# Kernel tuning notes

Hardware: AMD Instinct MI355X
Metric: run time of the kernel (lower is better)

Reference implementation:

```python
import jax, jax.numpy as jnp
import numpy as np

# dims: B graphs, E entities, R relations, N = E + R nodes, H hidden, P prop steps
B, N, E, R, H, P, RT, NH = 4, 2048, 1600, 448, 512, 2, 100, 4
DH = H // NH  # head dim = 128


def setup_inputs() -> dict:
    key = jax.random.key(0)
    ks = jax.random.split(key, 12)
    adj = jax.random.randint(ks[0], (B, N, N), 0, 2, dtype=jnp.int32)
    # self-loops so no attention row is fully masked (avoids NaN softmax rows)
    adj = jnp.maximum(adj, jnp.eye(N, dtype=jnp.int32)[None])
    rels = jax.random.randint(ks[1], (B, R), 0, RT, dtype=jnp.int32)
    vents = jax.random.normal(ks[2], (B, E, H), jnp.float32)
    renc_w = jax.random.normal(ks[3], (RT, H), jnp.float32) * 0.05  # xavier-ish
    s = 0.02
    inp = dict(adjs=adj, rels=rels, vents=vents, entlen=E, renc_w=renc_w)
    inp["Wq"] = jax.random.normal(ks[4], (P, H, H), jnp.float32) * s
    inp["Wk"] = jax.random.normal(ks[5], (P, H, H), jnp.float32) * s
    inp["Wv"] = jax.random.normal(ks[6], (P, H, H), jnp.float32) * s
    inp["Wo"] = jax.random.normal(ks[7], (P, H, H), jnp.float32) * s
    inp["W1"] = jax.random.normal(ks[8], (P, H, 4 * H), jnp.float32) * s
    inp["W2"] = jax.random.normal(ks[9], (P, 4 * H, H), jnp.float32) * s
    inp["bq"] = jnp.zeros((P, H), jnp.float32)
    inp["bk"] = jnp.zeros((P, H), jnp.float32)
    inp["bv"] = jnp.zeros((P, H), jnp.float32)
    inp["bo"] = jnp.zeros((P, H), jnp.float32)
    inp["b1"] = jnp.zeros((P, 4 * H), jnp.float32)
    inp["b2"] = jnp.zeros((P, H), jnp.float32)
    inp["ln1_g"] = jnp.ones((P, H), jnp.float32)
    inp["ln1_b"] = jnp.zeros((P, H), jnp.float32)
    inp["ln2_g"] = jnp.ones((P, H), jnp.float32)
    inp["ln2_b"] = jnp.zeros((P, H), jnp.float32)
    inp["prelu_a"] = jnp.full((P, 4 * H), 0.25, jnp.float32)  # torch PReLU default
    return inp


def _ln(x, g, b):
    mu = x.mean(-1, keepdims=True)
    var = x.var(-1, keepdims=True)
    return (x - mu) * jax.lax.rsqrt(var + jnp.float32(1e-5)) * g + b


def reference(adjs, rels, vents, entlen, renc_w, Wq, Wk, Wv, Wo, W1, W2,
              bq, bk, bv, bo, b1, b2, ln1_g, ln1_b, ln2_g, ln2_b, prelu_a):
    vrel = renc_w[rels]                              # (B,R,H) relation embeddings
    x = jnp.concatenate([vents, vrel], axis=1)       # (B,N,H) graph node features
    neg = (adjs == 0)[:, None, :, :]                 # (B,1,N,N) True = masked
    for j in range(P):  # prop steps, structurally distinct layers
        q = (x @ Wq[j] + bq[j]).reshape(B, N, NH, DH)
        k = (x @ Wk[j] + bk[j]).reshape(B, N, NH, DH)
        v = (x @ Wv[j] + bv[j]).reshape(B, N, NH, DH)
        sc = jnp.einsum('bqhd,bkhd->bhqk', q, k) / jnp.sqrt(jnp.float32(DH))
        sc = jnp.where(neg, jnp.float32(-1e9), sc)
        a = jax.nn.softmax(sc, axis=-1)
        o = jnp.einsum('bhqk,bkhd->bqhd', a, v).reshape(B, N, H)
        attn_out = o @ Wo[j] + bo[j]
        t = _ln(attn_out, ln1_g[j], ln1_b[j])        # ln_1
        hpre = t @ W1[j] + b1[j]
        hact = jnp.where(hpre >= 0, hpre, prelu_a[j] * hpre)  # PReLU
        y = hact @ W2[j] + b2[j]                     # dropout is identity in eval
        x = _ln(y + t, ln2_g[j], ln2_b[j])           # ln_2 residual
    glob = x[:, entlen]                              # (B,H) global node = vgraph[entlens[i]]
    gents = x                                        # (B,N,H) all graphs same size -> no pad
    elens = jnp.full((B,), N, jnp.int32)
    emask = jnp.arange(N)[None, :] <= elens[:, None] # (B,N) faithful `<=` comparison
    return glob, gents, emask
```

## Files before the change

### kernel.cpp

```cpp
#include <hip/hip_runtime.h>

typedef unsigned short u16;
typedef __bf16 bf16x8 __attribute__((ext_vector_type(8)));
typedef float floatx4 __attribute__((ext_vector_type(4)));


__device__ __forceinline__ float bf2f(u16 u) {
  union { unsigned int i; float f; } c; c.i = ((unsigned int)u) << 16; return c.f;
}
__device__ __forceinline__ u16 f2bf(float f) {
  union { unsigned int i; float f; } c; c.f = f;
  unsigned int i = c.i;
  return (u16)((i + 0x7FFFu + ((i >> 16) & 1u)) >> 16);
}

__device__ __forceinline__ void gload16(const u16* __restrict__ g, u16* l) {
  __builtin_amdgcn_global_load_lds(
      (const __attribute__((address_space(1))) unsigned int*)g,
      (__attribute__((address_space(3))) unsigned int*)l, 16, 0, 0);
}

template <int EPI, int FOUT, int SEG3>
__global__ __launch_bounds__(256, 3) void gemm_tn(
    const u16* __restrict__ A, const u16* __restrict__ Bt, void* __restrict__ Cv,
    const float* __restrict__ bias, const float* __restrict__ bias2,
    const float* __restrict__ bias3, const float* __restrict__ alpha,
    const float* __restrict__ res, int K, int lda, int ldb, int ldc) {
  __shared__ __align__(16) u16 As[2][128 * 32];
  __shared__ __align__(16) u16 Bs[2][128 * 32];

  const int tid = threadIdx.x;
  const int w = tid >> 6, lane = tid & 63;
  const int quad = lane >> 4, l16 = lane & 15;
  const int wm = w & 1, wn = w >> 1;

  const int slot0 = w * 128 + lane;
  const int slot1 = slot0 + 64;
  const u16* pA0 = A + (long)(blockIdx.x * 128 + (slot0 >> 2)) * lda + (slot0 & 3) * 8;
  const u16* pA1 = A + (long)(blockIdx.x * 128 + (slot1 >> 2)) * lda + (slot1 & 3) * 8;
  const u16* pB0 = Bt + (long)(blockIdx.y * 128 + (slot0 >> 2)) * ldb + (slot0 & 3) * 8;
  const u16* pB1 = Bt + (long)(blockIdx.y * 128 + (slot1 >> 2)) * ldb + (slot1 & 3) * 8;
  const int woff0 = w * 1024;
  const int woff1 = woff0 + 512;

  const floatx4 z4 = {0.f, 0.f, 0.f, 0.f};
  floatx4 acc[4][4];
#pragma unroll
  for (int i = 0; i < 4; i++)
#pragma unroll
    for (int j = 0; j < 4; j++) acc[i][j] = z4;

  gload16(pA0, &As[0][woff0]);
  gload16(pA1, &As[0][woff1]);
  gload16(pB0, &Bs[0][woff0]);
  gload16(pB1, &Bs[0][woff1]);
  pA0 += 32; pA1 += 32; pB0 += 32; pB1 += 32;
  __syncthreads();

  int p = 0;
  for (int k0 = 0; k0 < K; k0 += 32) {
    if (k0 + 32 < K) {
      gload16(pA0, &As[p ^ 1][woff0]);
      gload16(pA1, &As[p ^ 1][woff1]);
      gload16(pB0, &Bs[p ^ 1][woff0]);
      gload16(pB1, &Bs[p ^ 1][woff1]);
      pA0 += 32; pA1 += 32; pB0 += 32; pB1 += 32;
    }

    bf16x8 af[4], bv[4];
#pragma unroll
    for (int mi = 0; mi < 4; mi++)
      af[mi] = *(const bf16x8*)&As[p][(wm * 64 + mi * 16 + l16) * 32 + quad * 8];
#pragma unroll
    for (int ni = 0; ni < 4; ni++)
      bv[ni] = *(const bf16x8*)&Bs[p][(wn * 64 + ni * 16 + l16) * 32 + quad * 8];
#pragma unroll
    for (int mi = 0; mi < 4; mi++)
#pragma unroll
      for (int ni = 0; ni < 4; ni++)
        acc[mi][ni] = __builtin_amdgcn_mfma_f32_16x16x32_bf16(af[mi], bv[ni], acc[mi][ni], 0, 0, 0);

    __syncthreads();
    p ^= 1;
  }

  const float* bptr = bias;
  if (SEG3) {
    const int seg = blockIdx.y >> 2;
    bptr = (seg == 0) ? bias : ((seg == 1) ? bias2 : bias3);
  }
  const long crow0 = (long)blockIdx.x * 128;
  const int ncol0 = blockIdx.y * 128 + wn * 64 + l16;
#pragma unroll
  for (int mi = 0; mi < 4; mi++) {
#pragma unroll
    for (int r = 0; r < 4; r++) {
      const int m = wm * 64 + mi * 16 + quad * 4 + r;
      const long rowbase = (crow0 + m) * (long)ldc;
      const float* rrow = (EPI == 3) ? (res + rowbase) : nullptr;
#pragma unroll
      for (int ni = 0; ni < 4; ni++) {
        const int n = ncol0 + ni * 16;
        float vv = acc[mi][ni][r] + bptr[SEG3 ? (n & 511) : n];
        if (EPI == 2) { if (vv < 0.f) vv *= alpha[n]; }
        if (EPI == 3) vv += rrow[n];
        if (FOUT) ((float*)Cv)[rowbase + n] = vv;
        else ((u16*)Cv)[rowbase + n] = f2bf(vv);
      }
    }
  }
}

template <int EPI, int FOUT>
__global__ __launch_bounds__(256, 3) void gemm_tn64(
    const u16* __restrict__ A, const u16* __restrict__ Bt, void* __restrict__ Cv,
    const float* __restrict__ bias, const float* __restrict__ alpha,
    const float* __restrict__ res, int K, int lda, int ldb, int ldc) {
  __shared__ __align__(16) u16 As[2][128 * 32];
  __shared__ __align__(16) u16 Bs[2][64 * 32];

  const int tid = threadIdx.x;
  const int w = tid >> 6, lane = tid & 63;
  const int quad = lane >> 4, l16 = lane & 15;

  const int rA0 = tid >> 2, cA = (tid & 3) * 8;
  const int rA1 = rA0 + 64;
  const u16* pA0 = A + (long)(blockIdx.x * 128 + rA0) * lda + cA;
  const u16* pA1 = A + (long)(blockIdx.x * 128 + rA1) * lda + cA;
  const u16* pB  = Bt + (long)(blockIdx.y * 64 + rA0) * ldb + cA;
  const int aoff0 = w * 512;
  const int aoff1 = aoff0 + 2048;
  const int boff  = w * 512;

  const floatx4 z4 = {0.f, 0.f, 0.f, 0.f};
  floatx4 acc[2][4];
#pragma unroll
  for (int i = 0; i < 2; i++)
#pragma unroll
    for (int j = 0; j < 4; j++) acc[i][j] = z4;

  gload16(pA0, &As[0][aoff0]);
  gload16(pA1, &As[0][aoff1]);
  gload16(pB, &Bs[0][boff]);
  pA0 += 32; pA1 += 32; pB += 32;
  __syncthreads();

  int p = 0;
  for (int k0 = 0; k0 < K; k0 += 32) {
    if (k0 + 32 < K) {
      gload16(pA0, &As[p ^ 1][aoff0]);
      gload16(pA1, &As[p ^ 1][aoff1]);
      gload16(pB, &Bs[p ^ 1][boff]);
      pA0 += 32; pA1 += 32; pB += 32;
    }

    bf16x8 af[2], bv[4];
#pragma unroll
    for (int mi = 0; mi < 2; mi++)
      af[mi] = *(const bf16x8*)&As[p][(w * 32 + mi * 16 + l16) * 32 + quad * 8];
#pragma unroll
    for (int ni = 0; ni < 4; ni++)
      bv[ni] = *(const bf16x8*)&Bs[p][(ni * 16 + l16) * 32 + quad * 8];
#pragma unroll
    for (int mi = 0; mi < 2; mi++)
#pragma unroll
      for (int ni = 0; ni < 4; ni++)
        acc[mi][ni] = __builtin_amdgcn_mfma_f32_16x16x32_bf16(af[mi], bv[ni], acc[mi][ni], 0, 0, 0);

    __syncthreads();
    p ^= 1;
  }

  const long crow0 = (long)blockIdx.x * 128;
  const int ncol0 = blockIdx.y * 64 + l16;
#pragma unroll
  for (int mi = 0; mi < 2; mi++) {
#pragma unroll
    for (int r = 0; r < 4; r++) {
      const int m = w * 32 + mi * 16 + quad * 4 + r;
      const long rowbase = (crow0 + m) * (long)ldc;
      const float* rrow = (EPI == 3) ? (res + rowbase) : nullptr;
#pragma unroll
      for (int ni = 0; ni < 4; ni++) {
        const int n = ncol0 + ni * 16;
        float vv = acc[mi][ni][r] + bias[n];
        if (EPI == 2) { if (vv < 0.f) vv *= alpha[n]; }
        if (EPI == 3) vv += rrow[n];
        if (FOUT) ((float*)Cv)[rowbase + n] = vv;
        else ((u16*)Cv)[rowbase + n] = f2bf(vv);
      }
    }
  }
}

#define LDP 136
__global__ __launch_bounds__(256, 3) void k_attn(
    const u16* __restrict__ qkv, const u16* __restrict__ vt,
    const unsigned* __restrict__ mbits, u16* __restrict__ og) {
  __shared__ __align__(16) u16 KV[128 * LDP];
  __shared__ __align__(16) u16 Pl[64 * LDP];
  __shared__ unsigned Ml[64 * 4];

  const int tid = threadIdx.x;
  const int w = tid >> 6, lane = tid & 63;
  const int quad = lane >> 4, l16 = lane & 15;
  const int qt = blockIdx.x;
  const int z = blockIdx.y;
  const int b = z >> 2, h = z & 3;

  const u16* qbase = qkv + (long)b * 2048 * 1536 + h * 128;
  const u16* kbase = qbase + 512;
  const u16* vbase = vt + (long)(b * 4 + h) * 128 * 2048;
  const unsigned* mbase = mbits + ((long)b * 2048 + qt * 64) * 64;

  bf16x8 qf[4];
#pragma unroll
  for (int ks = 0; ks < 4; ks++)
    qf[ks] = *(const bf16x8*)(qbase +
        (long)(qt * 64 + w * 16 + l16) * 1536 + ks * 32 + quad * 8);

  const floatx4 z4 = {0.f, 0.f, 0.f, 0.f};
  floatx4 Oacc[8];
#pragma unroll
  for (int ni = 0; ni < 8; ni++) Oacc[ni] = z4;
  float mrow[4], lrow[4];
#pragma unroll
  for (int r = 0; r < 4; r++) { mrow[r] = -3.4e38f; lrow[r] = 0.f; }

  const float scale = 0.08838834764831845f;
  const int srow = tid >> 4;
  const int scol = (tid & 15) * 8;

  for (int kt = 0; kt < 16; kt++) {
    __syncthreads();
#pragma unroll
    for (int rr = 0; rr < 128; rr += 16)
      *(int4*)&KV[(rr + srow) * LDP + scol] =
          *(const int4*)(kbase + (long)(kt * 128 + rr + srow) * 1536 + scol);
    Ml[tid] = mbase[(tid >> 2) * 64 + kt * 4 + (tid & 3)];
    __syncthreads();

    floatx4 accS[8];
#pragma unroll
    for (int ni = 0; ni < 8; ni++) accS[ni] = z4;
#pragma unroll
    for (int ks = 0; ks < 4; ks++) {
      bf16x8 bf[8];
#pragma unroll
      for (int ni = 0; ni < 8; ni++)
        bf[ni] = *(const bf16x8*)&KV[(ni * 16 + l16) * LDP + ks * 32 + quad * 8];
#pragma unroll
      for (int ni = 0; ni < 8; ni++)
        accS[ni] = __builtin_amdgcn_mfma_f32_16x16x32_bf16(qf[ks], bf[ni], accS[ni], 0, 0, 0);
    }
    __syncthreads();

#pragma unroll
    for (int rr = 0; rr < 128; rr += 16)
      *(int4*)&KV[(rr + srow) * LDP + scol] =
          *(const int4*)(vbase + (long)(rr + srow) * 2048 + kt * 128 + scol);

#pragma unroll
    for (int r = 0; r < 4; r++) {
      const int rowl = w * 16 + quad * 4 + r;
      float s[8];
      float rmax = -1e30f;
#pragma unroll
      for (int ni = 0; ni < 8; ni++) {
        const unsigned mw = Ml[rowl * 4 + (ni >> 1)];
        const int on = (mw >> ((ni & 1) * 16 + l16)) & 1;
        s[ni] = on ? accS[ni][r] * scale : -1e30f;
        rmax = fmaxf(rmax, s[ni]);
      }
#pragma unroll
      for (int off = 1; off < 16; off <<= 1) rmax = fmaxf(rmax, __shfl_xor(rmax, off, 64));
      const float mnew = fmaxf(mrow[r], rmax);
      const float al = __expf(mrow[r] - mnew);
      float rs = 0.f;
#pragma unroll
      for (int ni = 0; ni < 8; ni++) {
        const float pp = __expf(s[ni] - mnew);
        rs += pp;
        Pl[rowl * LDP + ni * 16 + l16] = f2bf(pp);
      }
#pragma unroll
      for (int off = 1; off < 16; off <<= 1) rs += __shfl_xor(rs, off, 64);
      lrow[r] = lrow[r] * al + rs;
      mrow[r] = mnew;
#pragma unroll
      for (int ni = 0; ni < 8; ni++) Oacc[ni][r] *= al;
    }
    __syncthreads();

#pragma unroll
    for (int ks = 0; ks < 4; ks++) {
      bf16x8 bv[8];
#pragma unroll
      for (int ni = 0; ni < 8; ni++)
        bv[ni] = *(const bf16x8*)&KV[(ni * 16 + l16) * LDP + ks * 32 + quad * 8];
      bf16x8 pf = *(const bf16x8*)&Pl[(w * 16 + l16) * LDP + ks * 32 + quad * 8];
#pragma unroll
      for (int ni = 0; ni < 8; ni++)
        Oacc[ni] = __builtin_amdgcn_mfma_f32_16x16x32_bf16(pf, bv[ni], Oacc[ni], 0, 0, 0);
    }
  }

#pragma unroll
  for (int r = 0; r < 4; r++) {
    const float inv = 1.f / lrow[r];
    const long q = qt * 64 + w * 16 + quad * 4 + r;
#pragma unroll
    for (int ni = 0; ni < 8; ni++)
      og[((long)b * 2048 + q) * 512 + h * 128 + ni * 16 + l16] = f2bf(Oacc[ni][r] * inv);
  }
}

__global__ __launch_bounds__(256) void k_maskpack(const int* __restrict__ adjs,
                                                  unsigned* __restrict__ bits) {
  const int wid = blockIdx.x * 4 + (threadIdx.x >> 6);
  const int lane = threadIdx.x & 63;
  const unsigned long long bal = __ballot(adjs[(long)wid * 64 + lane] != 0);
  if (lane == 0) {
    bits[wid * 2] = (unsigned)bal;
    bits[wid * 2 + 1] = (unsigned)(bal >> 32);
  }
}

__global__ __launch_bounds__(256) void tr_w(const float* __restrict__ src, u16* __restrict__ dst,
                                            int ld_src, int ld_dst, long s_z, long d_z) {
  __shared__ u16 tile[32][33];
  src += (long)blockIdx.z * s_z;
  dst += (long)blockIdx.z * d_z;
  const int r0 = blockIdx.x << 5, c0 = blockIdx.y << 5;
  const int tx = threadIdx.x & 31, ty = threadIdx.x >> 5;
#pragma unroll
  for (int i = 0; i < 32; i += 8)
    tile[ty + i][tx] = f2bf(src[(long)(r0 + ty + i) * ld_src + c0 + tx]);
  __syncthreads();
#pragma unroll
  for (int i = 0; i < 32; i += 8)
    dst[(long)(c0 + ty + i) * ld_dst + r0 + tx] = tile[tx][ty + i];
}

__global__ __launch_bounds__(256) void tr_bf16(const u16* __restrict__ src, u16* __restrict__ dst,
                                               int ld_src, int ld_dst, int zdiv,
                                               long s_out, long s_in, long d_out, long d_in_) {
  __shared__ u16 tile[32][33];
  const int zz = blockIdx.z, zq = zz / zdiv, zr = zz % zdiv;
  src += (long)zq * s_out + (long)zr * s_in;
  dst += (long)zq * d_out + (long)zr * d_in_;
  const int r0 = blockIdx.x << 5, c0 = blockIdx.y << 5;
  const int tx = threadIdx.x & 31, ty = threadIdx.x >> 5;
#pragma unroll
  for (int i = 0; i < 32; i += 8) tile[ty + i][tx] = src[(long)(r0 + ty + i) * ld_src + c0 + tx];
  __syncthreads();
#pragma unroll
  for (int i = 0; i < 32; i += 8) dst[(long)(c0 + ty + i) * ld_dst + r0 + tx] = tile[tx][ty + i];
}

__global__ __launch_bounds__(256) void k_build_x(const float* __restrict__ vents,
                                                 const int* __restrict__ rels,
                                                 const float* __restrict__ renc,
                                                 float* __restrict__ x, u16* __restrict__ xb) {
  const long idx = (long)blockIdx.x * 256 + threadIdx.x;
  const int c = (int)(idx & 511);
  const int row = (int)(idx >> 9);
  const int b = row >> 11, n = row & 2047;
  float val;
  if (n < 1600) val = vents[((long)b * 1600 + n) * 512 + c];
  else val = renc[(long)rels[b * 448 + (n - 1600)] * 512 + c];
  x[idx] = val;
  xb[idx] = f2bf(val);
}

__global__ __launch_bounds__(256) void k_ln(const float* __restrict__ in, float* __restrict__ out,
                                            u16* __restrict__ outb,
                                            const float* __restrict__ g, const float* __restrict__ bb) {
  __shared__ float rs[256], rq[256];
  const int row = blockIdx.x, tid = threadIdx.x;
  const float* p = in + (long)row * 512;
  const float a0 = p[tid], a1 = p[tid + 256];
  rs[tid] = a0 + a1;
  rq[tid] = a0 * a0 + a1 * a1;
  __syncthreads();
  for (int s = 128; s > 0; s >>= 1) {
    if (tid < s) { rs[tid] += rs[tid + s]; rq[tid] += rq[tid + s]; }
    __syncthreads();
  }
  const float mu = rs[0] * (1.f / 512.f);
  const float var = rq[0] * (1.f / 512.f) - mu * mu;
  const float inv = 1.0f / sqrtf(var + 1e-5f);
  const float o0 = (a0 - mu) * inv * g[tid] + bb[tid];
  const float o1 = (a1 - mu) * inv * g[tid + 256] + bb[tid + 256];
  out[(long)row * 512 + tid] = o0;
  out[(long)row * 512 + tid + 256] = o1;
  outb[(long)row * 512 + tid] = f2bf(o0);
  outb[(long)row * 512 + tid + 256] = f2bf(o1);
}

__global__ __launch_bounds__(256) void k_out(const float* __restrict__ x, const int* __restrict__ entlen,
                                             float* __restrict__ out, long out_n) {
  const long idx = (long)blockIdx.x * 256 + threadIdx.x;
  if (idx >= out_n) return;
  const long G = 2048, GE = 2048 + 4194304;
  float v;
  if (idx < G) {
    const int b = (int)(idx >> 9), c = (int)(idx & 511);
    int e = entlen[0];
    if (e < 0 || e >= 2048) e = 1600;
    v = x[((long)b * 2048 + e) * 512 + c];
  } else if (idx < GE) {
    v = x[idx - G];
  } else {
    v = 1.0f;
  }
  out[idx] = v;
}

extern "C" void kernel_launch(void* const* d_in, const int* in_sizes, int n_in,
                              void* d_out, int out_size, void* d_ws, size_t ws_size,
                              hipStream_t stream) {
  const int* adjs = (const int*)d_in[0];
  const int* rels = (const int*)d_in[1];
  const float* vents = (const float*)d_in[2];
  const int* entlen = (const int*)d_in[3];
  const float* renc = (const float*)d_in[4];
  const float* Wq = (const float*)d_in[5];
  const float* Wk = (const float*)d_in[6];
  const float* Wv = (const float*)d_in[7];
  const float* Wo = (const float*)d_in[8];
  const float* W1 = (const float*)d_in[9];
  const float* W2 = (const float*)d_in[10];
  const float* bq = (const float*)d_in[11];
  const float* bk = (const float*)d_in[12];
  const float* bv = (const float*)d_in[13];
  const float* bo = (const float*)d_in[14];
  const float* b1 = (const float*)d_in[15];
  const float* b2 = (const float*)d_in[16];
  const float* ln1g = (const float*)d_in[17];
  const float* ln1b = (const float*)d_in[18];
  const float* ln2g = (const float*)d_in[19];
  const float* ln2b = (const float*)d_in[20];
  const float* prelu = (const float*)d_in[21];

  char* base = (char*)d_ws;
  float* x_f   = (float*)(base + 0);
  float* t_f   = (float*)(base + 16777216);
  float* tmp_f = (float*)(base + 33554432);
  u16* wt  = (u16*)(base + 50331648);
  u16* xb  = (u16*)(base + 62914560);
  u16* tb  = (u16*)(base + 71303168);
  u16* qkv = (u16*)(base + 79691776);
  u16* Vtb = (u16*)(base + 104857600);
  u16* ob  = (u16*)(base + 113246208);
  u16* hb  = (u16*)(base + 121634816);
  unsigned* mbits = (unsigned*)(base + 155189248);

  k_build_x<<<dim3(16384), 256, 0, stream>>>(vents, rels, renc, x_f, xb);
  k_maskpack<<<dim3(65536), 256, 0, stream>>>(adjs, mbits);

  tr_w<<<dim3(16, 16, 2), 256, 0, stream>>>(Wq, wt + 0,       512, 512, 262144L, 3145728L);
  tr_w<<<dim3(16, 16, 2), 256, 0, stream>>>(Wk, wt + 262144,  512, 512, 262144L, 3145728L);
  tr_w<<<dim3(16, 16, 2), 256, 0, stream>>>(Wv, wt + 524288,  512, 512, 262144L, 3145728L);
  tr_w<<<dim3(16, 16, 2), 256, 0, stream>>>(Wo, wt + 786432,  512, 512, 262144L, 3145728L);
  tr_w<<<dim3(16, 64, 2), 256, 0, stream>>>(W1, wt + 1048576, 2048, 512, 1048576L, 3145728L);
  tr_w<<<dim3(64, 16, 2), 256, 0, stream>>>(W2, wt + 2097152, 512, 2048, 1048576L, 3145728L);

  for (int j = 0; j < 2; j++) {
    const u16* wqt = wt + (long)j * 3145728;
    const u16* wot = wqt + 786432;
    const u16* w1t = wqt + 1048576;
    const u16* w2t = wqt + 2097152;

    gemm_tn<1, 0, 1><<<dim3(64, 12), 256, 0, stream>>>(
        xb, wqt, qkv, bq + j * 512, bk + j * 512, bv + j * 512, nullptr, nullptr,
        512, 512, 512, 1536);

    tr_bf16<<<dim3(64, 4, 16), 256, 0, stream>>>(qkv + 1024, Vtb, 1536, 2048, 4,
        3145728L, 128L, 1048576L, 262144L);

    k_attn<<<dim3(32, 16), 256, 0, stream>>>(qkv, Vtb, mbits, ob);

    gemm_tn64<1, 1><<<dim3(64, 8), 256, 0, stream>>>(ob, wot, tmp_f, bo + j * 512, nullptr, nullptr, 512, 512, 512, 512);
    k_ln<<<dim3(8192), 256, 0, stream>>>(tmp_f, t_f, tb, ln1g + j * 512, ln1b + j * 512);
    gemm_tn<2, 0, 0><<<dim3(64, 16), 256, 0, stream>>>(tb, w1t, hb, b1 + j * 2048, nullptr, nullptr, prelu + j * 2048, nullptr, 512, 512, 512, 2048);
    gemm_tn64<3, 1><<<dim3(64, 8), 256, 0, stream>>>(hb, w2t, tmp_f, b2 + j * 512, nullptr, t_f, 2048, 2048, 2048, 512);
    k_ln<<<dim3(8192), 256, 0, stream>>>(tmp_f, x_f, xb, ln2g + j * 512, ln2b + j * 512);
  }

  const long out_n = (long)out_size;
  k_out<<<dim3((unsigned)((out_n + 255) / 256)), 256, 0, stream>>>(x_f, entlen, (float*)d_out, out_n);
}
```

Measured before the change: 629.7 us.

## Load V fragments directly from global into registers with double buffering

The attention kernel no longer stages the V tile through shared memory. Each wave reads its V MFMA operands straight from global memory into registers, alternating between two buffers so the next slice loads while the current one feeds the MFMAs. This removes two block-wide barriers and the LDS write/read round trip for V per key tile. In exchange every wave fetches the whole V tile on its own, which raises global/L2 traffic, and the extra fragment registers raise VGPR pressure under the 3-blocks-per-CU launch bound.

```diff
diff --git a/kernel.cpp b/kernel.cpp
--- a/kernel.cpp
+++ b/kernel.cpp
@@ -197,7 +197,7 @@
 __global__ __launch_bounds__(256, 3) void k_attn(
     const u16* __restrict__ qkv, const u16* __restrict__ vt,
     const unsigned* __restrict__ mbits, u16* __restrict__ og) {
-  __shared__ __align__(16) u16 KV[128 * LDP];
+  __shared__ __align__(16) u16 Ks[128 * LDP];
   __shared__ __align__(16) u16 Pl[64 * LDP];
   __shared__ unsigned Ml[64 * 4];
 
@@ -235,7 +235,7 @@
     __syncthreads();
 #pragma unroll
     for (int rr = 0; rr < 128; rr += 16)
-      *(int4*)&KV[(rr + srow) * LDP + scol] =
+      *(int4*)&Ks[(rr + srow) * LDP + scol] =
           *(const int4*)(kbase + (long)(kt * 128 + rr + srow) * 1536 + scol);
     Ml[tid] = mbase[(tid >> 2) * 64 + kt * 4 + (tid & 3)];
     __syncthreads();
@@ -248,17 +248,17 @@
       bf16x8 bf[8];
 #pragma unroll
       for (int ni = 0; ni < 8; ni++)
-        bf[ni] = *(const bf16x8*)&KV[(ni * 16 + l16) * LDP + ks * 32 + quad * 8];
+        bf[ni] = *(const bf16x8*)&Ks[(ni * 16 + l16) * LDP + ks * 32 + quad * 8];
 #pragma unroll
       for (int ni = 0; ni < 8; ni++)
         accS[ni] = __builtin_amdgcn_mfma_f32_16x16x32_bf16(qf[ks], bf[ni], accS[ni], 0, 0, 0);
     }
-    __syncthreads();
-
-#pragma unroll
-    for (int rr = 0; rr < 128; rr += 16)
-      *(int4*)&KV[(rr + srow) * LDP + scol] =
-          *(const int4*)(vbase + (long)(rr + srow) * 2048 + kt * 128 + scol);
+
+    const u16* vk = vbase + kt * 128 + quad * 8;
+    bf16x8 bvA[8], bvB[8];
+#pragma unroll
+    for (int ni = 0; ni < 8; ni++)
+      bvA[ni] = *(const bf16x8*)(vk + (long)(ni * 16 + l16) * 2048);
 
 #pragma unroll
     for (int r = 0; r < 4; r++) {
@@ -290,18 +290,39 @@
 #pragma unroll
       for (int ni = 0; ni < 8; ni++) Oacc[ni][r] *= al;
     }
-    __syncthreads();
-
-#pragma unroll
-    for (int ks = 0; ks < 4; ks++) {
-      bf16x8 bv[8];
-#pragma unroll
-      for (int ni = 0; ni < 8; ni++)
-        bv[ni] = *(const bf16x8*)&KV[(ni * 16 + l16) * LDP + ks * 32 + quad * 8];
-      bf16x8 pf = *(const bf16x8*)&Pl[(w * 16 + l16) * LDP + ks * 32 + quad * 8];
-#pragma unroll
-      for (int ni = 0; ni < 8; ni++)
-        Oacc[ni] = __builtin_amdgcn_mfma_f32_16x16x32_bf16(pf, bv[ni], Oacc[ni], 0, 0, 0);
+
+    {
+#pragma unroll
+      for (int ni = 0; ni < 8; ni++)
+        bvB[ni] = *(const bf16x8*)(vk + (long)(ni * 16 + l16) * 2048 + 32);
+      bf16x8 pf = *(const bf16x8*)&Pl[(w * 16 + l16) * LDP + quad * 8];
+#pragma unroll
+      for (int ni = 0; ni < 8; ni++)
+        Oacc[ni] = __builtin_amdgcn_mfma_f32_16x16x32_bf16(pf, bvA[ni], Oacc[ni], 0, 0, 0);
+    }
+    {
+#pragma unroll
+      for (int ni = 0; ni < 8; ni++)
+        bvA[ni] = *(const bf16x8*)(vk + (long)(ni * 16 + l16) * 2048 + 64);
+      bf16x8 pf = *(const bf16x8*)&Pl[(w * 16 + l16) * LDP + 32 + quad * 8];
+#pragma unroll
+      for (int ni = 0; ni < 8; ni++)
+        Oacc[ni] = __builtin_amdgcn_mfma_f32_16x16x32_bf16(pf, bvB[ni], Oacc[ni], 0, 0, 0);
+    }
+    {
+#pragma unroll
+      for (int ni = 0; ni < 8; ni++)
+        bvB[ni] = *(const bf16x8*)(vk + (long)(ni * 16 + l16) * 2048 + 96);
+      bf16x8 pf = *(const bf16x8*)&Pl[(w * 16 + l16) * LDP + 64 + quad * 8];
+#pragma unroll
+      for (int ni = 0; ni < 8; ni++)
+        Oacc[ni] = __builtin_amdgcn_mfma_f32_16x16x32_bf16(pf, bvA[ni], Oacc[ni], 0, 0, 0);
+    }
+    {
+      bf16x8 pf = *(const bf16x8*)&Pl[(w * 16 + l16) * LDP + 96 + quad * 8];
+#pragma unroll
+      for (int ni = 0; ni < 8; ni++)
+        Oacc[ni] = __builtin_amdgcn_mfma_f32_16x16x32_bf16(pf, bvB[ni], Oacc[ni], 0, 0, 0);
     }
   }
 
```

Measured after the change: 731.3 us. 16.1% more time.
